# Kernel optimization log

Hardware: AMD Instinct MI355X
Metric: run time of the kernel (lower is better)

The kernel has to match this reference:

```python
import jax, jax.numpy as jnp
import numpy as np

D_MODEL = 1024
N_HEADS = 16
N_PHASE = 128
HEAD_DIM = D_MODEL // N_HEADS
PHASE_PER_HEAD = N_PHASE // N_HEADS
CONTENT_SCALE = 1.0 / np.sqrt(HEAD_DIM)
PHASE_SCALE = 1.0 / np.sqrt(PHASE_PER_HEAD)
LN_EPS = 1e-5


def create_position_phases(L, n_phase, base=10000.0):
    # RoPE-style: each freq repeated at even/odd indices (interleaved)
    inv_freq = 1.0 / base ** (jnp.arange(0, n_phase, 2, dtype=jnp.float32) / n_phase)
    pos = jnp.arange(L, dtype=jnp.float32)
    sinusoid = pos[:, None] * inv_freq[None, :]          # (L, n_phase//2)
    return jnp.repeat(sinusoid, 2, axis=1)               # (L, n_phase)


def setup_inputs() -> dict:
    key = jax.random.key(0)
    ks = jax.random.split(key, 12)
    B, L, D, P = 1, 2048, D_MODEL, N_PHASE
    s = 0.02
    return {
        'x_real': jax.random.normal(ks[0], (B, L, D), jnp.float32),
        'x_imag': jax.random.normal(ks[1], (B, L, D), jnp.float32),
        'Wq': jax.random.normal(ks[2], (D, D), jnp.float32) * s,
        'Wk': jax.random.normal(ks[3], (D, D), jnp.float32) * s,
        'Wv': jax.random.normal(ks[4], (D, D), jnp.float32) * s,
        'Wqp': jax.random.normal(ks[5], (D, P), jnp.float32) * s,
        'bqp': jax.random.uniform(ks[6], (P,), jnp.float32, -np.pi, np.pi),
        'Wkp': jax.random.normal(ks[7], (D, P), jnp.float32) * s,
        'bkp': jax.random.uniform(ks[8], (P,), jnp.float32, -np.pi, np.pi),
        'Wo': jax.random.normal(ks[9], (D, D), jnp.float32) * s,
        'alpha_logit': jnp.zeros((N_HEADS, 1, 1), jnp.float32),
        'ln_gamma': jnp.ones((D,), jnp.float32),
        'ln_beta': jnp.zeros((D,), jnp.float32),
    }


def _split_heads(x, B, L, H, hd):
    return x.reshape(B, L, H, hd).transpose(0, 2, 1, 3)  # (B,H,L,hd)


def reference(x_real, x_imag, Wq, Wk, Wv, Wqp, bqp, Wkp, bkp, Wo,
              alpha_logit, ln_gamma, ln_beta):
    B, L, D = x_real.shape
    H, hd, p = N_HEADS, HEAD_DIM, PHASE_PER_HEAD

    Q = _split_heads(x_real @ Wq, B, L, H, hd)
    K = _split_heads(x_real @ Wk, B, L, H, hd)
    V = _split_heads(x_real @ Wv, B, L, H, hd)
    content = jnp.einsum('bhqd,bhkd->bhqk', Q, K) * CONTENT_SCALE

    pos_phase = create_position_phases(L, N_PHASE)        # (L, P)
    Qt = _split_heads(x_imag @ Wqp + bqp + pos_phase, B, L, H, p)
    Kt = _split_heads(x_imag @ Wkp + bkp + pos_phase, B, L, H, p)
    phase = (jnp.einsum('bhqp,bhkp->bhqk', jnp.cos(Qt), jnp.cos(Kt))
             + jnp.einsum('bhqp,bhkp->bhqk', jnp.sin(Qt), jnp.sin(Kt))) * PHASE_SCALE

    alpha = jax.nn.sigmoid(alpha_logit)                   # (H,1,1) broadcasts over (B,H,L,L)
    scores = (1.0 - alpha) * content + alpha * phase

    causal = jnp.triu(jnp.ones((L, L), bool), 1)
    scores = jnp.where(causal, -jnp.inf, scores)
    attn = jax.nn.softmax(scores, axis=-1)

    out = jnp.einsum('bhqk,bhkd->bhqd', attn, V)
    out = out.transpose(0, 2, 1, 3).reshape(B, L, D) @ Wo

    h = x_real + out
    mu = jnp.mean(h, axis=-1, keepdims=True)
    var = jnp.var(h, axis=-1, keepdims=True)
    out_real = (h - mu) / jnp.sqrt(var + LN_EPS) * ln_gamma + ln_beta
    return out_real, x_imag
```

## Files before the change

### kernel.cpp

```cpp
#include <hip/hip_runtime.h>
#include <hip/hip_bf16.h>
#include <math.h>

#define L 2048
#define D 1024
#define NH 16
#define HD 64
#define P 128
#define HDE 96
#define CONTENT_SCALE 0.125f
#define PHASE_SCALE   0.35355339059327373f
#define KLS 104
#define VT2 136
#define NSPLIT 2

typedef short bf16x8 __attribute__((ext_vector_type(8)));
typedef float f32x4 __attribute__((ext_vector_type(4)));
typedef float f32x16 __attribute__((ext_vector_type(16)));

__device__ inline ushort f2b(float x) {
    __hip_bfloat16 b = __float2bfloat16(x);
    return *(ushort*)&b;
}
__device__ inline float b2f(ushort u) {
    unsigned v = (unsigned)u << 16;
    union { unsigned u; float f; } c; c.u = v; return c.f;
}

__device__ inline void sincos_hw(float ang, float* sn, float* cs) {
    float rev = ang * 0.15915494309189535f;
    rev -= floorf(rev);
    *sn = __builtin_amdgcn_sinf(rev);
    *cs = __builtin_amdgcn_cosf(rev);
}

__device__ inline void gld_lds16(const void* g, void* l) {
    __builtin_amdgcn_global_load_lds(
        (const __attribute__((address_space(1))) unsigned int*)g,
        (__attribute__((address_space(3))) unsigned int*)l,
        16, 0, 0);
}

__global__ void prep_kernel(const float* __restrict__ xr, const float* __restrict__ xi,
                            ushort* __restrict__ xrb, ushort* __restrict__ xib,
                            const float* __restrict__ W0, const float* __restrict__ W1,
                            const float* __restrict__ W2, const float* __restrict__ W3,
                            const float* __restrict__ W4, const float* __restrict__ W5,
                            ushort* __restrict__ T0, ushort* __restrict__ T1,
                            ushort* __restrict__ T2, ushort* __restrict__ T3,
                            ushort* __restrict__ Tp,
                            ushort* __restrict__ Qe, ushort* __restrict__ Ke) {
    __shared__ float tile[32][33];
    const int b = blockIdx.x;
    const int tid = threadIdx.x;
    if (b < 4096) {
        const float4* src = (b >> 11) ? (const float4*)xi : (const float4*)xr;
        ushort4* dst = (b >> 11) ? (ushort4*)xib : (ushort4*)xrb;
        int i = ((b & 2047) << 8) + tid;
        float4 v = src[i];
        ushort4 o;
        o.x = f2b(v.x); o.y = f2b(v.y); o.z = f2b(v.z); o.w = f2b(v.w);
        dst[i] = o;
    } else if (b < 8448) {
        int w = b - 4096;
        const float* W; ushort* T; int ncols, n0, k0;
        if (w < 4096) {
            int z = w >> 10, t = w & 1023;
            n0 = (t & 31) * 32; k0 = (t >> 5) * 32; ncols = D;
            W = (z == 0) ? W0 : ((z == 1) ? W1 : ((z == 2) ? W2 : W3));
            T = (z == 0) ? T0 : ((z == 1) ? T1 : ((z == 2) ? T2 : T3));
        } else {
            int w2 = w - 4096;
            int z = w2 >> 7, t = w2 & 127;
            n0 = (t & 3) * 32; k0 = (t >> 2) * 32; ncols = P;
            W = z ? W5 : W4;
            T = Tp + (size_t)z * P * D;
        }
        int tx = tid & 31, ty = tid >> 5;
#pragma unroll
        for (int i = 0; i < 4; i++)
            tile[ty + i * 8][tx] = W[(size_t)(k0 + ty + i * 8) * ncols + n0 + tx];
        __syncthreads();
#pragma unroll
        for (int i = 0; i < 4; i++)
            T[(size_t)(n0 + ty + i * 8) * D + k0 + tx] = f2b(tile[tx][ty + i * 8]);
    } else {
        int i = (b - 8448) * 256 + tid;
        size_t base = (size_t)i * HDE + 80;
        uint4 z4 = make_uint4(0, 0, 0, 0);
        *(uint4*)(Qe + base) = z4;
        *(uint4*)(Qe + base + 8) = z4;
        *(uint4*)(Ke + base) = z4;
        *(uint4*)(Ke + base + 8) = z4;
    }
}

__launch_bounds__(256)
__global__ void qkv_gemm(const ushort* __restrict__ Ab, const ushort* __restrict__ xib,
                         const ushort* __restrict__ Wtq, const ushort* __restrict__ Wtk,
                         const ushort* __restrict__ Wtv, const ushort* __restrict__ Wtp,
                         ushort* __restrict__ Qe, ushort* __restrict__ Ke,
                         ushort* __restrict__ Ve, const float* __restrict__ alpha,
                         const float* __restrict__ bqp, const float* __restrict__ bkp) {
    const int z = blockIdx.z;
    if (z == 3 && blockIdx.x >= 2) return;
    const ushort* At = (z == 3) ? xib : Ab;
    const ushort* Bt = (z == 0) ? Wtq : ((z == 1) ? Wtk : ((z == 2) ? Wtv : Wtp));
    __shared__ ushort As0[128 * 32], Bs0[128 * 32];
    __shared__ ushort As1[128 * 32], Bs1[128 * 32];
    const int tid = threadIdx.x;
    const int wave = tid >> 6, lane = tid & 63, quad = lane >> 4, ln16 = lane & 15;
    const int wm = wave >> 1, wn = wave & 1;
    const int m0 = blockIdx.y * 128, n0 = blockIdx.x * 128;
    f32x4 acc[4][4];
#pragma unroll
    for (int i = 0; i < 4; i++)
#pragma unroll
        for (int j = 0; j < 4; j++) acc[i][j] = (f32x4){0.f, 0.f, 0.f, 0.f};

    auto stage = [&](int kt, ushort* Asb, ushort* Bsb) {
#pragma unroll
        for (int i = 0; i < 2; i++) {
            int idx = i * 256 + tid;
            int r2 = idx >> 2, cc = idx & 3;
            gld_lds16(At + (size_t)(m0 + r2) * D + kt + cc * 8, &Asb[idx * 8]);
            gld_lds16(Bt + (size_t)(n0 + r2) * D + kt + cc * 8, &Bsb[idx * 8]);
        }
    };
    auto compute = [&](const ushort* Asb, const ushort* Bsb) {
        bf16x8 af[4], bfr[4];
#pragma unroll
        for (int t = 0; t < 4; t++) {
            af[t]  = *(const bf16x8*)(&Asb[(wm * 64 + t * 16 + ln16) * 32 + quad * 8]);
            bfr[t] = *(const bf16x8*)(&Bsb[(wn * 64 + t * 16 + ln16) * 32 + quad * 8]);
        }
#pragma unroll
        for (int i = 0; i < 4; i++)
#pragma unroll
            for (int j = 0; j < 4; j++)
                acc[i][j] = __builtin_amdgcn_mfma_f32_16x16x32_bf16(af[i], bfr[j], acc[i][j], 0, 0, 0);
    };

    stage(0, As0, Bs0);
    __syncthreads();
    for (int kt = 0; kt < D; kt += 64) {
        stage(kt + 32, As1, Bs1);
        compute(As0, Bs0);
        __syncthreads();
        if (kt + 64 < D) stage(kt + 64, As0, Bs0);
        compute(As1, Bs1);
        __syncthreads();
    }

    if (z == 2) {
        int hn = (n0 + wn * 64) >> 6;
#pragma unroll
        for (int i = 0; i < 4; i++)
#pragma unroll
            for (int j = 0; j < 4; j++) {
                int d = j * 16 + ln16;
                int m = m0 + wm * 64 + i * 16 + quad * 4;
                ushort4 pk;
                pk.x = f2b(acc[i][j][0]); pk.y = f2b(acc[i][j][1]);
                pk.z = f2b(acc[i][j][2]); pk.w = f2b(acc[i][j][3]);
                *(ushort4*)(Ve + ((size_t)hn * HD + d) * L + m) = pk;
            }
    } else if (z < 2) {
        int hn = (n0 + wn * 64) >> 6;
        float s = (z == 0) ? (1.f - 1.f / (1.f + __expf(-alpha[hn]))) * CONTENT_SCALE : 1.f;
        ushort* dst = (z == 0) ? Qe : Ke;
#pragma unroll
        for (int i = 0; i < 4; i++)
#pragma unroll
            for (int j = 0; j < 4; j++) {
                int dcol = j * 16 + ln16;
#pragma unroll
                for (int r = 0; r < 4; r++) {
                    int m = m0 + wm * 64 + i * 16 + quad * 4 + r;
                    dst[((size_t)hn * L + m) * HDE + dcol] = f2b(acc[i][j][r] * s);
                }
            }
    } else {
#pragma unroll
        for (int j = 0; j < 4; j++) {
            int cg = n0 + wn * 64 + j * 16 + ln16;
            int isQ = cg < P;
            int c = cg & (P - 1);
            int hh = c >> 3, jj = c & 7;
            float b = isQ ? bqp[c] : bkp[c];
            float sc = isQ ? (1.f / (1.f + __expf(-alpha[hh]))) * PHASE_SCALE : 1.f;
            float invf = __expf(-((float)(c & ~1) / 128.f) * 9.210340371976184f);
            ushort* dst = isQ ? Qe : Ke;
#pragma unroll
            for (int i = 0; i < 4; i++)
#pragma unroll
                for (int r = 0; r < 4; r++) {
                    int m = m0 + wm * 64 + i * 16 + quad * 4 + r;
                    float qt = acc[i][j][r] + b + (float)m * invf;
                    float sn, cs;
                    sincos_hw(qt, &sn, &cs);
                    size_t base = ((size_t)hh * L + m) * HDE;
                    dst[base + 64 + jj] = f2b(sc * cs);
                    dst[base + 72 + jj] = f2b(sc * sn);
                }
        }
    }
}

__launch_bounds__(256, 2)
__global__ void flash_attn(const ushort* __restrict__ Qe, const ushort* __restrict__ Ke,
                           const ushort* __restrict__ Vte,
                           ushort* __restrict__ Opart, float* __restrict__ ml) {
    const int b = blockIdx.x;
    const int xcd = b & 7;
    const int r = b >> 3;
    const int idx = r & 31, sub = r >> 5;
    const int hbit = idx >> 4, c0i = idx & 15;
    const int c = sub ? 15 - c0i : c0i;
    const int z = sub;
    const int h = xcd * 2 + hbit;
    const int tid = threadIdx.x;
    const int wave = tid >> 6, lane = tid & 63;
    const int ln32 = lane & 31, hf = lane >> 5;

    const int nT = c + 1;
    const int s0 = z * nT;
    const int nR = (nT + 1) >> 1;
    const int qw = c * 128 + wave * 32;

    __shared__ ushort Kl[128 * KLS];
    __shared__ ushort Vt[64 * VT2];

    const ushort* Kh = Ke + (size_t)h * L * HDE;
    const ushort* Vh = Vte + (size_t)h * HD * L;
    const ushort* Qh = Qe + (size_t)h * L * HDE;
    ushort* Op = Opart + (size_t)z * L * D;
    float* mlp = ml + (size_t)z * NH * L + (size_t)h * L;

    bf16x8 onesv;
#pragma unroll
    for (int i = 0; i < 8; i++) onesv[i] = (short)0x3F80;

    bf16x8 qa[6];
#pragma unroll
    for (int cc = 0; cc < 6; cc++)
        qa[cc] = *(const bf16x8*)(Qh + (size_t)(qw + ln32) * HDE + cc * 16 + hf * 8);

    f32x16 o[2], olv;
#pragma unroll
    for (int i = 0; i < 16; i++) { o[0][i] = 0.f; o[1][i] = 0.f; olv[i] = 0.f; }

    int rowk[6], colk[6];
#pragma unroll
    for (int ii = 0; ii < 6; ii++) {
        int ix = ii * 256 + tid;
        rowk[ii] = ix / 12; colk[ii] = ix - rowk[ii] * 12;
    }
    int dv[4], cv[4];
#pragma unroll
    for (int ii = 0; ii < 4; ii++) {
        int ix = ii * 256 + tid;
        dv[ii] = ix >> 4; cv[ii] = ix & 15;
    }

    bf16x8 kreg[6], vreg[4];
    {
        int kk = s0 * 64;
#pragma unroll
        for (int ii = 0; ii < 6; ii++)
            kreg[ii] = *(const bf16x8*)(Kh + (size_t)(kk + rowk[ii]) * HDE + colk[ii] * 8);
#pragma unroll
        for (int ii = 0; ii < 4; ii++)
            vreg[ii] = *(const bf16x8*)(Vh + (size_t)dv[ii] * L + kk + cv[ii] * 8);
    }

    for (int rr = 0; rr < nR; rr++) {
        const int tk0 = (s0 + rr * 2) * 64;
        __syncthreads();
#pragma unroll
        for (int ii = 0; ii < 6; ii++)
            *(bf16x8*)(&Kl[rowk[ii] * KLS + colk[ii] * 8]) = kreg[ii];
#pragma unroll
        for (int ii = 0; ii < 4; ii++)
            *(bf16x8*)(&Vt[dv[ii] * VT2 + cv[ii] * 8]) = vreg[ii];
        __syncthreads();

        if (rr + 1 < nR) {
            int kk = tk0 + 128;
#pragma unroll
            for (int ii = 0; ii < 6; ii++)
                kreg[ii] = *(const bf16x8*)(Kh + (size_t)(kk + rowk[ii]) * HDE + colk[ii] * 8);
#pragma unroll
            for (int ii = 0; ii < 4; ii++)
                vreg[ii] = *(const bf16x8*)(Vh + (size_t)dv[ii] * L + kk + cv[ii] * 8);
        }

#pragma unroll
        for (int hb = 0; hb < 2; hb++) {
            const int tt = rr * 2 + hb;
            const int k0 = tk0 + hb * 64;
            if (tt < nT && k0 < qw + 32) {
                f32x16 s2[2];
#pragma unroll
                for (int i = 0; i < 16; i++) { s2[0][i] = 0.f; s2[1][i] = 0.f; }
                __builtin_amdgcn_s_setprio(1);
#pragma unroll
                for (int kb = 0; kb < 2; kb++)
#pragma unroll
                    for (int cc = 0; cc < 6; cc++) {
                        bf16x8 kf = *(const bf16x8*)(&Kl[(hb * 64 + kb * 32 + ln32) * KLS + cc * 16 + hf * 8]);
                        s2[kb] = __builtin_amdgcn_mfma_f32_32x32x16_bf16(kf, qa[cc], s2[kb], 0, 0, 0);
                    }
                __builtin_amdgcn_s_setprio(0);

                if (k0 + 63 > qw) {
#pragma unroll
                    for (int kb = 0; kb < 2; kb++)
#pragma unroll
                        for (int rg = 0; rg < 16; rg++) {
                            int key = k0 + kb * 32 + (rg & 3) + 8 * (rg >> 2) + 4 * hf;
                            if (key > qw + ln32) s2[kb][rg] = -1e30f;
                        }
                }

#pragma unroll
                for (int kb = 0; kb < 2; kb++)
#pragma unroll
                    for (int rg = 0; rg < 16; rg++)
                        s2[kb][rg] = __expf(s2[kb][rg]);

                unsigned Xp[2][4], Yp[2][4];
#pragma unroll
                for (int kb = 0; kb < 2; kb++)
#pragma unroll
                    for (int tq = 0; tq < 4; tq++) {
                        asm("v_cvt_pk_bf16_f32 %0, %1, %2"
                            : "=v"(Xp[kb][tq]) : "v"(s2[kb][4 * tq + 0]), "v"(s2[kb][4 * tq + 1]));
                        asm("v_cvt_pk_bf16_f32 %0, %1, %2"
                            : "=v"(Yp[kb][tq]) : "v"(s2[kb][4 * tq + 2]), "v"(s2[kb][4 * tq + 3]));
                    }

                bf16x8 pa[4];
#pragma unroll
                for (int m = 0; m < 4; m++) {
                    int kb = m >> 1, te = 2 * (m & 1), to = te + 1;
                    unsigned x0 = Xp[kb][te], x1 = Xp[kb][to];
                    unsigned y0 = Yp[kb][te], y1 = Yp[kb][to];
                    asm("v_permlane32_swap_b32 %0, %1" : "+v"(x0), "+v"(x1));
                    asm("v_permlane32_swap_b32 %0, %1" : "+v"(y0), "+v"(y1));
                    union { unsigned u[4]; bf16x8 v; } pb;
                    pb.u[0] = x0; pb.u[1] = y0; pb.u[2] = x1; pb.u[3] = y1;
                    pa[m] = pb.v;
                }

                __builtin_amdgcn_s_setprio(1);
#pragma unroll
                for (int m = 0; m < 4; m++) {
#pragma unroll
                    for (int db = 0; db < 2; db++) {
                        bf16x8 vf = *(const bf16x8*)(&Vt[(db * 32 + ln32) * VT2 + hb * 64 + m * 16 + hf * 8]);
                        o[db] = __builtin_amdgcn_mfma_f32_32x32x16_bf16(pa[m], vf, o[db], 0, 0, 0);
                    }
                    olv = __builtin_amdgcn_mfma_f32_32x32x16_bf16(pa[m], onesv, olv, 0, 0, 0);
                }
                __builtin_amdgcn_s_setprio(0);
            }
        }
    }

    if (ln32 == 0) {
#pragma unroll
        for (int rg = 0; rg < 16; rg++) {
            int q = qw + (rg & 3) + 8 * (rg >> 2) + 4 * hf;
            mlp[q] = olv[rg];
        }
    }
#pragma unroll
    for (int db = 0; db < 2; db++)
#pragma unroll
        for (int rg = 0; rg < 16; rg++) {
            int q = qw + (rg & 3) + 8 * (rg >> 2) + 4 * hf;
            Op[(size_t)q * D + h * HD + db * 32 + ln32] = f2b(o[db][rg]);
        }
}

__global__ void comb_kernel(const ushort* __restrict__ Opart, const float* __restrict__ ml,
                            ushort* __restrict__ AOb) {
    int q = blockIdx.x;
    int t = threadIdx.x;
    int h = t >> 4;
    float lsum = 0.f;
#pragma unroll
    for (int zz = 0; zz < NSPLIT; zz++)
        lsum += ml[(size_t)zz * NH * L + (size_t)h * L + q];
    float inv = 1.f / lsum;
    size_t idx = (size_t)q * D + t * 4;
    float ox = 0.f, oy = 0.f, oz = 0.f, ow = 0.f;
#pragma unroll
    for (int zz = 0; zz < NSPLIT; zz++) {
        ushort4 a = *(const ushort4*)(Opart + (size_t)zz * L * D + idx);
        ox += b2f(a.x); oy += b2f(a.y); oz += b2f(a.z); ow += b2f(a.w);
    }
    ushort4 o;
    o.x = f2b(ox * inv); o.y = f2b(oy * inv);
    o.z = f2b(oz * inv); o.w = f2b(ow * inv);
    *(ushort4*)(AOb + idx) = o;
}

__launch_bounds__(256)
__global__ void wo_gemm(const ushort* __restrict__ Ab, const ushort* __restrict__ Bt,
                        float* __restrict__ C) {
    __shared__ ushort As0[128 * 32], Bs0[64 * 32];
    __shared__ ushort As1[128 * 32], Bs1[64 * 32];
    const int tid = threadIdx.x;
    const int wave = tid >> 6, lane = tid & 63, quad = lane >> 4, ln16 = lane & 15;
    const int m0 = blockIdx.y * 128, n0 = blockIdx.x * 64;
    f32x4 acc[2][4];
#pragma unroll
    for (int i = 0; i < 2; i++)
#pragma unroll
        for (int j = 0; j < 4; j++) acc[i][j] = (f32x4){0.f, 0.f, 0.f, 0.f};

    auto stage = [&](int kt, ushort* Asb, ushort* Bsb) {
#pragma unroll
        for (int i = 0; i < 2; i++) {
            int idx = i * 256 + tid;
            int r2 = idx >> 2, cc = idx & 3;
            gld_lds16(Ab + (size_t)(m0 + r2) * D + kt + cc * 8, &Asb[idx * 8]);
        }
        {
            int r2 = tid >> 2, cc = tid & 3;
            gld_lds16(Bt + (size_t)(n0 + r2) * D + kt + cc * 8, &Bsb[tid * 8]);
        }
    };
    auto compute = [&](const ushort* Asb, const ushort* Bsb) {
        bf16x8 af[2], bfr[4];
#pragma unroll
        for (int i = 0; i < 2; i++)
            af[i] = *(const bf16x8*)(&Asb[(wave * 32 + i * 16 + ln16) * 32 + quad * 8]);
#pragma unroll
        for (int j = 0; j < 4; j++)
            bfr[j] = *(const bf16x8*)(&Bsb[(j * 16 + ln16) * 32 + quad * 8]);
#pragma unroll
        for (int i = 0; i < 2; i++)
#pragma unroll
            for (int j = 0; j < 4; j++)
                acc[i][j] = __builtin_amdgcn_mfma_f32_16x16x32_bf16(af[i], bfr[j], acc[i][j], 0, 0, 0);
    };

    stage(0, As0, Bs0);
    __syncthreads();
    for (int kt = 0; kt < D; kt += 64) {
        stage(kt + 32, As1, Bs1);
        compute(As0, Bs0);
        __syncthreads();
        if (kt + 64 < D) stage(kt + 64, As0, Bs0);
        compute(As1, Bs1);
        __syncthreads();
    }
#pragma unroll
    for (int i = 0; i < 2; i++)
#pragma unroll
        for (int j = 0; j < 4; j++)
#pragma unroll
            for (int r = 0; r < 4; r++) {
                int m = m0 + wave * 32 + i * 16 + quad * 4 + r;
                int n = n0 + j * 16 + ln16;
                C[(size_t)m * D + n] = acc[i][j][r];
            }
}

__global__ void ln_kernel(const float* __restrict__ xr, const float* __restrict__ o2,
                          const float* __restrict__ gamma, const float* __restrict__ beta,
                          float* __restrict__ outp, const float4* __restrict__ xi4,
                          float4* __restrict__ out1) {
    int l = blockIdx.x;
    int tid = threadIdx.x;
    int wave = tid >> 6;
    __shared__ float red[8];
    float hv[4];
    float s = 0.f;
#pragma unroll
    for (int i = 0; i < 4; i++) {
        int c = tid + i * 256;
        hv[i] = xr[(size_t)l * D + c] + o2[(size_t)l * D + c];
        s += hv[i];
    }
    out1[(size_t)l * (D / 4) + tid] = xi4[(size_t)l * (D / 4) + tid];
#pragma unroll
    for (int off = 1; off < 64; off <<= 1) s += __shfl_xor(s, off);
    if ((tid & 63) == 0) red[wave] = s;
    __syncthreads();
    float mu = (red[0] + red[1] + red[2] + red[3]) * (1.f / D);
    float v = 0.f;
#pragma unroll
    for (int i = 0; i < 4; i++) { float d = hv[i] - mu; v += d * d; }
#pragma unroll
    for (int off = 1; off < 64; off <<= 1) v += __shfl_xor(v, off);
    __syncthreads();
    if ((tid & 63) == 0) red[4 + wave] = v;
    __syncthreads();
    float rstd = rsqrtf((red[4] + red[5] + red[6] + red[7]) * (1.f / D) + 1e-5f);
#pragma unroll
    for (int i = 0; i < 4; i++) {
        int c = tid + i * 256;
        outp[(size_t)l * D + c] = (hv[i] - mu) * rstd * gamma[c] + beta[c];
    }
}

extern "C" void kernel_launch(void* const* d_in, const int* in_sizes, int n_in,
                              void* d_out, int out_size, void* d_ws, size_t ws_size,
                              hipStream_t stream) {
    const float* xr    = (const float*)d_in[0];
    const float* xi    = (const float*)d_in[1];
    const float* Wq    = (const float*)d_in[2];
    const float* Wk    = (const float*)d_in[3];
    const float* Wv    = (const float*)d_in[4];
    const float* Wqp   = (const float*)d_in[5];
    const float* bqp   = (const float*)d_in[6];
    const float* Wkp   = (const float*)d_in[7];
    const float* bkp   = (const float*)d_in[8];
    const float* Wo    = (const float*)d_in[9];
    const float* alpha = (const float*)d_in[10];
    const float* gamma = (const float*)d_in[11];
    const float* beta  = (const float*)d_in[12];

    const size_t LD = (size_t)L * D;
    const size_t MB = 1024 * 1024;

    char* A8 = (char*)d_out;
    char* B8 = A8 + LD * 4;
    ushort* xib = (ushort*)A8;
    ushort* AOb = (ushort*)A8;
    ushort* Wot = (ushort*)(A8 + 4 * MB);
    ushort* Wtq = (ushort*)(A8 + 6 * MB);
    ushort* xrb = (ushort*)B8;
    ushort* Wtk = (ushort*)(B8 + 4 * MB);
    ushort* Wtv = (ushort*)(B8 + 6 * MB);
    float* outf = (float*)d_out;

    ushort* Qe = (ushort*)d_ws;
    ushort* Ke = Qe + (size_t)NH * L * HDE;
    ushort* Ve = Ke + (size_t)NH * L * HDE;
    ushort* Wqpkt = Ve + (size_t)NH * L * HD;
    ushort* Opart = Wqpkt + (size_t)256 * D;
    float*  mlbuf = (float*)(Opart + (size_t)NSPLIT * LD);
    float*  O2 = (float*)d_ws;

    prep_kernel<<<8576, 256, 0, stream>>>(xr, xi, xrb, xib,
                                          Wq, Wk, Wv, Wo, Wqp, Wkp,
                                          Wtq, Wtk, Wtv, Wot, Wqpkt, Qe, Ke);

    qkv_gemm<<<dim3(8, 16, 4), 256, 0, stream>>>(xrb, xib, Wtq, Wtk, Wtv, Wqpkt,
                                                 Qe, Ke, Ve, alpha, bqp, bkp);

    flash_attn<<<512, 256, 0, stream>>>(Qe, Ke, Ve, Opart, mlbuf);

    comb_kernel<<<L, 256, 0, stream>>>(Opart, mlbuf, AOb);

    wo_gemm<<<dim3(16, 16), 256, 0, stream>>>(AOb, Wot, O2);

    ln_kernel<<<L, 256, 0, stream>>>(xr, O2, gamma, beta, outf,
                                     (const float4*)xi, (float4*)(B8));
}
```

Measured before the change: 180.5 us.

## Swizzle GEMM LDS layout and use 8-wave blocks in QKV projection

The QKV GEMM goes from 4 to 8 waves per block, each wave computing a 64x32 sub-tile instead of 64x64. Each thread now issues one global-to-LDS load per operand per stage. Both the QKV and Wo GEMMs XOR-swizzle the 16-byte column chunk index by row when writing and reading LDS, to avoid bank conflicts on the fragment loads. In exchange, each wave does less MFMA work per LDS fragment read, and each 512-thread block holds more registers.

```diff
diff --git a/kernel.cpp b/kernel.cpp
--- a/kernel.cpp
+++ b/kernel.cpp
@@ -95,7 +95,7 @@
     }
 }
 
-__launch_bounds__(256)
+__launch_bounds__(512)
 __global__ void qkv_gemm(const ushort* __restrict__ Ab, const ushort* __restrict__ xib,
                          const ushort* __restrict__ Wtq, const ushort* __restrict__ Wtk,
                          const ushort* __restrict__ Wtv, const ushort* __restrict__ Wtp,
@@ -110,34 +110,34 @@
     __shared__ ushort As1[128 * 32], Bs1[128 * 32];
     const int tid = threadIdx.x;
     const int wave = tid >> 6, lane = tid & 63, quad = lane >> 4, ln16 = lane & 15;
-    const int wm = wave >> 1, wn = wave & 1;
+    const int wm = wave >> 2, wn = wave & 3;
     const int m0 = blockIdx.y * 128, n0 = blockIdx.x * 128;
-    f32x4 acc[4][4];
+    f32x4 acc[4][2];
 #pragma unroll
     for (int i = 0; i < 4; i++)
 #pragma unroll
-        for (int j = 0; j < 4; j++) acc[i][j] = (f32x4){0.f, 0.f, 0.f, 0.f};
+        for (int j = 0; j < 2; j++) acc[i][j] = (f32x4){0.f, 0.f, 0.f, 0.f};
+
+    const int r2 = tid >> 2, cc = tid & 3;
+    const int cc2 = cc ^ ((r2 >> 1) & 3);
+    const int swr = (ln16 >> 1) & 3;
 
     auto stage = [&](int kt, ushort* Asb, ushort* Bsb) {
-#pragma unroll
-        for (int i = 0; i < 2; i++) {
-            int idx = i * 256 + tid;
-            int r2 = idx >> 2, cc = idx & 3;
-            gld_lds16(At + (size_t)(m0 + r2) * D + kt + cc * 8, &Asb[idx * 8]);
-            gld_lds16(Bt + (size_t)(n0 + r2) * D + kt + cc * 8, &Bsb[idx * 8]);
-        }
+        gld_lds16(At + (size_t)(m0 + r2) * D + kt + cc2 * 8, &Asb[tid * 8]);
+        gld_lds16(Bt + (size_t)(n0 + r2) * D + kt + cc2 * 8, &Bsb[tid * 8]);
     };
     auto compute = [&](const ushort* Asb, const ushort* Bsb) {
-        bf16x8 af[4], bfr[4];
-#pragma unroll
-        for (int t = 0; t < 4; t++) {
-            af[t]  = *(const bf16x8*)(&Asb[(wm * 64 + t * 16 + ln16) * 32 + quad * 8]);
-            bfr[t] = *(const bf16x8*)(&Bsb[(wn * 64 + t * 16 + ln16) * 32 + quad * 8]);
-        }
+        bf16x8 af[4], bfr[2];
+#pragma unroll
+        for (int t = 0; t < 4; t++)
+            af[t] = *(const bf16x8*)(&Asb[(wm * 64 + t * 16 + ln16) * 32 + (quad ^ swr) * 8]);
+#pragma unroll
+        for (int j = 0; j < 2; j++)
+            bfr[j] = *(const bf16x8*)(&Bsb[(wn * 32 + j * 16 + ln16) * 32 + (quad ^ swr) * 8]);
 #pragma unroll
         for (int i = 0; i < 4; i++)
 #pragma unroll
-            for (int j = 0; j < 4; j++)
+            for (int j = 0; j < 2; j++)
                 acc[i][j] = __builtin_amdgcn_mfma_f32_16x16x32_bf16(af[i], bfr[j], acc[i][j], 0, 0, 0);
     };
 
@@ -153,12 +153,12 @@
     }
 
     if (z == 2) {
-        int hn = (n0 + wn * 64) >> 6;
+        int hn = (n0 >> 6) + (wn >> 1);
 #pragma unroll
         for (int i = 0; i < 4; i++)
 #pragma unroll
-            for (int j = 0; j < 4; j++) {
-                int d = j * 16 + ln16;
+            for (int j = 0; j < 2; j++) {
+                int d = (wn & 1) * 32 + j * 16 + ln16;
                 int m = m0 + wm * 64 + i * 16 + quad * 4;
                 ushort4 pk;
                 pk.x = f2b(acc[i][j][0]); pk.y = f2b(acc[i][j][1]);
@@ -166,14 +166,14 @@
                 *(ushort4*)(Ve + ((size_t)hn * HD + d) * L + m) = pk;
             }
     } else if (z < 2) {
-        int hn = (n0 + wn * 64) >> 6;
+        int hn = (n0 >> 6) + (wn >> 1);
         float s = (z == 0) ? (1.f - 1.f / (1.f + __expf(-alpha[hn]))) * CONTENT_SCALE : 1.f;
         ushort* dst = (z == 0) ? Qe : Ke;
 #pragma unroll
         for (int i = 0; i < 4; i++)
 #pragma unroll
-            for (int j = 0; j < 4; j++) {
-                int dcol = j * 16 + ln16;
+            for (int j = 0; j < 2; j++) {
+                int dcol = (wn & 1) * 32 + j * 16 + ln16;
 #pragma unroll
                 for (int r = 0; r < 4; r++) {
                     int m = m0 + wm * 64 + i * 16 + quad * 4 + r;
@@ -182,8 +182,8 @@
             }
     } else {
 #pragma unroll
-        for (int j = 0; j < 4; j++) {
-            int cg = n0 + wn * 64 + j * 16 + ln16;
+        for (int j = 0; j < 2; j++) {
+            int cg = n0 + wn * 32 + j * 16 + ln16;
             int isQ = cg < P;
             int c = cg & (P - 1);
             int hh = c >> 3, jj = c & 7;
@@ -415,6 +415,7 @@
     const int tid = threadIdx.x;
     const int wave = tid >> 6, lane = tid & 63, quad = lane >> 4, ln16 = lane & 15;
     const int m0 = blockIdx.y * 128, n0 = blockIdx.x * 64;
+    const int swr = (ln16 >> 1) & 3;
     f32x4 acc[2][4];
 #pragma unroll
     for (int i = 0; i < 2; i++)
@@ -426,21 +427,23 @@
         for (int i = 0; i < 2; i++) {
             int idx = i * 256 + tid;
             int r2 = idx >> 2, cc = idx & 3;
-            gld_lds16(Ab + (size_t)(m0 + r2) * D + kt + cc * 8, &Asb[idx * 8]);
+            int cc2 = cc ^ ((r2 >> 1) & 3);
+            gld_lds16(Ab + (size_t)(m0 + r2) * D + kt + cc2 * 8, &Asb[idx * 8]);
         }
         {
             int r2 = tid >> 2, cc = tid & 3;
-            gld_lds16(Bt + (size_t)(n0 + r2) * D + kt + cc * 8, &Bsb[tid * 8]);
+            int cc2 = cc ^ ((r2 >> 1) & 3);
+            gld_lds16(Bt + (size_t)(n0 + r2) * D + kt + cc2 * 8, &Bsb[tid * 8]);
         }
     };
     auto compute = [&](const ushort* Asb, const ushort* Bsb) {
         bf16x8 af[2], bfr[4];
 #pragma unroll
         for (int i = 0; i < 2; i++)
-            af[i] = *(const bf16x8*)(&Asb[(wave * 32 + i * 16 + ln16) * 32 + quad * 8]);
+            af[i] = *(const bf16x8*)(&Asb[(wave * 32 + i * 16 + ln16) * 32 + (quad ^ swr) * 8]);
 #pragma unroll
         for (int j = 0; j < 4; j++)
-            bfr[j] = *(const bf16x8*)(&Bsb[(j * 16 + ln16) * 32 + quad * 8]);
+            bfr[j] = *(const bf16x8*)(&Bsb[(j * 16 + ln16) * 32 + (quad ^ swr) * 8]);
 #pragma unroll
         for (int i = 0; i < 2; i++)
 #pragma unroll
@@ -551,7 +554,7 @@
                                           Wq, Wk, Wv, Wo, Wqp, Wkp,
                                           Wtq, Wtk, Wtv, Wot, Wqpkt, Qe, Ke);
 
-    qkv_gemm<<<dim3(8, 16, 4), 256, 0, stream>>>(xrb, xib, Wtq, Wtk, Wtv, Wqpkt,
+    qkv_gemm<<<dim3(8, 16, 4), 512, 0, stream>>>(xrb, xib, Wtq, Wtk, Wtv, Wqpkt,
                                                  Qe, Ke, Ve, alpha, bqp, bkp);
 
     flash_attn<<<512, 256, 0, stream>>>(Qe, Ke, Ve, Opart, mlbuf);
```

After: 176.9 us. 2.0% less time.
